# Optimization experiments

Hardware: AMD Instinct MI355X
Metric: run time of the kernel (lower is better)

The kernel has to match this reference:

```python
import jax, jax.numpy as jnp
import numpy as np

B, T, C, H = 2, 2048, 1024, 16
D = C // H  # head dim = 64
EPS = 1e-6  # kernel adds 1e-6 to softmax denominator


def setup_inputs() -> dict:
    key = jax.random.key(0)
    k1, k2, k3, k4, k5 = jax.random.split(key, 5)
    s = 1.0 / np.sqrt(C)
    return {
        "x": jax.random.normal(k1, (B, T, C), dtype=jnp.float32),
        "w_attn": jax.random.normal(k2, (3 * C, C), dtype=jnp.float32) * s,
        "b_attn": jax.random.normal(k3, (3 * C,), dtype=jnp.float32) * 0.02,
        "w_proj": jax.random.normal(k4, (C, C), dtype=jnp.float32) * s,
        "b_proj": jax.random.normal(k5, (C,), dtype=jnp.float32) * 0.02,
    }


def reference(x, w_attn, b_attn, w_proj, b_proj):
    b, t, c = x.shape
    qkv = x @ w_attn.T + b_attn                      # [B,T,3C]
    q, k, v = jnp.split(qkv, 3, axis=2)
    # [B,T,C] -> [B,H,T,D]
    q = q.reshape(b, t, H, D).transpose(0, 2, 1, 3)
    k = k.reshape(b, t, H, D).transpose(0, 2, 1, 3)
    v = v.reshape(b, t, H, D).transpose(0, 2, 1, 3)
    scale = 1.0 / np.sqrt(D)
    att = jnp.einsum("bhid,bhjd->bhij", q, k) * scale  # [B,H,T,T]
    causal = jnp.tril(jnp.ones((t, t), dtype=bool))
    att = jnp.where(causal, att, -jnp.inf)
    # softmax matching the HIP kernel: denom has +1e-6
    m = jnp.max(att, axis=-1, keepdims=True)
    e = jnp.exp(att - m)                             # masked entries -> 0
    p = e / (jnp.sum(e, axis=-1, keepdims=True) + EPS)
    y = jnp.einsum("bhij,bhjd->bhid", p, v)          # [B,H,T,D]
    y = y.transpose(0, 2, 1, 3).reshape(b, t, c)     # [B,T,C]
    return y @ w_proj.T + b_proj
```

## Files before the change

### kernel.cpp

```cpp
#include <hip/hip_runtime.h>

#define B_ 2
#define T_ 2048
#define C_ 1024
#define H_ 16
#define D_ 64

typedef __bf16 bf16x8 __attribute__((ext_vector_type(8)));
typedef float f32x4 __attribute__((ext_vector_type(4)));

__device__ __forceinline__ unsigned short f2bf(float f) {
  unsigned u = __float_as_uint(f);
  unsigned r = (u + 0x7fffu + ((u >> 16) & 1u)) >> 16;
  return (unsigned short)r;
}
__device__ __forceinline__ float bf2f(unsigned short u) {
  return __uint_as_float(((unsigned)u) << 16);
}

__global__ __launch_bounds__(256) void f32_to_bf16_kernel(
    const float* __restrict__ src, unsigned short* __restrict__ dst, int n4) {
  int i = blockIdx.x * 256 + threadIdx.x;
  if (i < n4) {
    float4 v = ((const float4*)src)[i];
    ushort4 u;
    u.x = f2bf(v.x); u.y = f2bf(v.y); u.z = f2bf(v.z); u.w = f2bf(v.w);
    ((ushort4*)dst)[i] = u;
  }
}

__global__ __launch_bounds__(256) void gemm_bt(
    const unsigned short* __restrict__ A,
    const unsigned short* __restrict__ Bm,
    const float* __restrict__ bias,
    int M, int N, int K, int mode,
    float* __restrict__ outf,
    unsigned short* __restrict__ qb,
    unsigned short* __restrict__ kb,
    unsigned short* __restrict__ vb) {
  __shared__ unsigned short As[128 * 64];
  __shared__ unsigned short Bs[128 * 64];

  const int tid  = threadIdx.x;
  const int lane = tid & 63;
  const int wave = tid >> 6;
  const int quad = lane >> 4;
  const int l16  = lane & 15;
  const int q4   = quad * 4;

  const int bm = blockIdx.y * 128;
  const int bn = blockIdx.x * 128;
  const int wm = (wave >> 1) * 64;
  const int wn = (wave & 1) * 64;

  f32x4 acc[4][4] = {};

  const int srow8 = lane >> 3;
  const int scol  = ((lane & 7) ^ srow8) * 8;
  const int srow  = wave * 8 + srow8;

  for (int k0 = 0; k0 < K; k0 += 64) {
#pragma unroll
    for (int c = 0; c < 4; ++c) {
      const int r = c * 32 + srow;
      const unsigned short* ga = A  + (size_t)(bm + r) * K + (k0 + scol);
      const unsigned short* gb = Bm + (size_t)(bn + r) * K + (k0 + scol);
      unsigned short* la = &As[(c * 32 + wave * 8) * 64];
      unsigned short* lb = &Bs[(c * 32 + wave * 8) * 64];
      __builtin_amdgcn_global_load_lds(
          (__attribute__((address_space(1))) unsigned int*)ga,
          (__attribute__((address_space(3))) unsigned int*)la, 16, 0, 0);
      __builtin_amdgcn_global_load_lds(
          (__attribute__((address_space(1))) unsigned int*)gb,
          (__attribute__((address_space(3))) unsigned int*)lb, 16, 0, 0);
    }
    __syncthreads();
#pragma unroll
    for (int ks = 0; ks < 2; ++ks) {
      bf16x8 af[4], bfr[4];
#pragma unroll
      for (int i = 0; i < 4; ++i)
        af[i] = *(const bf16x8*)&As[(wm + i * 16 + l16) * 64 +
                                    (((ks * 4 + quad) ^ (l16 & 7)) * 8)];
#pragma unroll
      for (int j = 0; j < 4; ++j)
        bfr[j] = *(const bf16x8*)&Bs[(wn + j * 16 + l16) * 64 +
                                     (((ks * 4 + quad) ^ (l16 & 7)) * 8)];
#pragma unroll
      for (int i = 0; i < 4; ++i)
#pragma unroll
        for (int j = 0; j < 4; ++j)
          acc[i][j] = __builtin_amdgcn_mfma_f32_16x16x32_bf16(af[i], bfr[j], acc[i][j], 0, 0, 0);
    }
    __syncthreads();
  }

#pragma unroll
  for (int j = 0; j < 4; ++j) {
    const int gn = bn + wn + j * 16 + l16;
    const float bv = bias[gn];
    if (mode == 0) {
#pragma unroll
      for (int i = 0; i < 4; ++i)
#pragma unroll
        for (int r = 0; r < 4; ++r) {
          const int gm = bm + wm + i * 16 + q4 + r;
          outf[(size_t)gm * N + gn] = acc[i][j][r] + bv;
        }
    } else {
      const int which = gn >> 10;
      const int cc = gn & 1023;
      const int h = cc >> 6, d = cc & 63;
      if (which == 2) {
#pragma unroll
        for (int i = 0; i < 4; ++i) {
          const int gm0 = bm + wm + i * 16 + q4;
          const int b = gm0 >> 11, t0 = gm0 & 2047;
          ushort4 u;
          u.x = f2bf(acc[i][j][0] + bv);
          u.y = f2bf(acc[i][j][1] + bv);
          u.z = f2bf(acc[i][j][2] + bv);
          u.w = f2bf(acc[i][j][3] + bv);
          *(ushort4*)&vb[(((size_t)(b * H_ + h) * D_) + d) * T_ + t0] = u;
        }
      } else {
        const float sc = (which == 0) ? 0.125f : 1.0f;
        unsigned short* dst = (which == 0) ? qb : kb;
#pragma unroll
        for (int i = 0; i < 4; ++i)
#pragma unroll
          for (int r = 0; r < 4; ++r) {
            const int gm = bm + wm + i * 16 + q4 + r;
            const int b = gm >> 11, t = gm & 2047;
            dst[(((size_t)(b * H_ + h) * T_) + t) * D_ + d] = f2bf((acc[i][j][r] + bv) * sc);
          }
      }
    }
  }
}

__global__ __launch_bounds__(256, 2) void attn_mfma(
    const unsigned short* __restrict__ Qb,
    const unsigned short* __restrict__ Kb,
    const unsigned short* __restrict__ Vtg,
    unsigned short* __restrict__ Yb) {
  __shared__ unsigned short Ks[64 * 64];
  __shared__ unsigned short Vt[64 * 64];
  __shared__ unsigned short Pw[4][32 * 64];

  const int tid  = threadIdx.x;
  const int lane = tid & 63;
  const int wave = tid >> 6;
  const int quad = lane >> 4;
  const int l16  = lane & 15;
  const int q4   = quad * 4;
  const int sw   = (l16 & 7);

  const int id = blockIdx.x;
  int bh, qt;
  if (id < 256) { bh = id & 31; qt = 15 - (id >> 5); }
  else          { bh = (id - 256) & 31; qt = (id - 256) >> 5; }
  const int b = bh >> 4, h = bh & 15;
  const size_t base = (size_t)bh * T_ * D_;

  const int wq = qt * 128 + wave * 32;

  bf16x8 qf[2][2];
#pragma unroll
  for (int nt = 0; nt < 2; ++nt)
#pragma unroll
    for (int ks = 0; ks < 2; ++ks)
      qf[nt][ks] = *(const bf16x8*)(Qb + base + (size_t)(wq + nt * 16 + l16) * 64 +
                                    ks * 32 + quad * 8);

  f32x4 o[4][2] = {};
  float l2[2] = {0.f, 0.f};

  const int ktiles = 2 * qt + 2;
  const int srow8 = lane >> 3;
  const int satom = ((lane & 7) ^ srow8) * 8;

  for (int kt = 0; kt < ktiles; ++kt) {
    const int kt0 = kt * 64;
    __syncthreads();
#pragma unroll
    for (int c = 0; c < 2; ++c) {
      const int row = wave * 16 + c * 8 + srow8;
      const unsigned short* gk = Kb  + base + (size_t)(kt0 + row) * 64 + satom;
      const unsigned short* gv = Vtg + base + (size_t)row * T_ + kt0 + satom;
      unsigned short* lk = &Ks[(wave * 16 + c * 8) * 64];
      unsigned short* lv = &Vt[(wave * 16 + c * 8) * 64];
      __builtin_amdgcn_global_load_lds(
          (__attribute__((address_space(1))) unsigned int*)gk,
          (__attribute__((address_space(3))) unsigned int*)lk, 16, 0, 0);
      __builtin_amdgcn_global_load_lds(
          (__attribute__((address_space(1))) unsigned int*)gv,
          (__attribute__((address_space(3))) unsigned int*)lv, 16, 0, 0);
    }
    __syncthreads();

    if (kt0 <= wq + 31) {
      f32x4 s[4][2] = {};
#pragma unroll
      for (int ks = 0; ks < 2; ++ks) {
        bf16x8 kf[4];
#pragma unroll
        for (int mt = 0; mt < 4; ++mt)
          kf[mt] = *(const bf16x8*)&Ks[(mt * 16 + l16) * 64 +
                                       (((ks * 4 + quad) ^ sw) * 8)];
#pragma unroll
        for (int mt = 0; mt < 4; ++mt)
#pragma unroll
          for (int nt = 0; nt < 2; ++nt)
            s[mt][nt] = __builtin_amdgcn_mfma_f32_16x16x32_bf16(kf[mt], qf[nt][ks],
                                                                s[mt][nt], 0, 0, 0);
      }
      if (kt0 + 63 > wq) {
#pragma unroll
        for (int mt = 0; mt < 4; ++mt)
#pragma unroll
          for (int nt = 0; nt < 2; ++nt)
#pragma unroll
            for (int r = 0; r < 4; ++r)
              if (kt0 + mt * 16 + q4 + r > wq + nt * 16 + l16) s[mt][nt][r] = -1e30f;
      }
#pragma unroll
      for (int nt = 0; nt < 2; ++nt) {
        float ps = 0.f;
#pragma unroll
        for (int mt = 0; mt < 4; ++mt) {
          float p0 = __expf(s[mt][nt][0]);
          float p1 = __expf(s[mt][nt][1]);
          float p2 = __expf(s[mt][nt][2]);
          float p3 = __expf(s[mt][nt][3]);
          ps += (p0 + p1) + (p2 + p3);
          unsigned lo = (unsigned)f2bf(p0) | ((unsigned)f2bf(p1) << 16);
          unsigned hi = (unsigned)f2bf(p2) | ((unsigned)f2bf(p3) << 16);
          uint2 pk; pk.x = lo; pk.y = hi;
          const int atom = (2 * mt + (quad >> 1)) ^ sw;
          *(uint2*)&Pw[wave][(nt * 16 + l16) * 64 + atom * 8 + (quad & 1) * 4] = pk;
        }
        l2[nt] += ps;
      }
#pragma unroll
      for (int ks = 0; ks < 2; ++ks) {
        bf16x8 vf[4], pf[2];
#pragma unroll
        for (int dt = 0; dt < 4; ++dt)
          vf[dt] = *(const bf16x8*)&Vt[(dt * 16 + l16) * 64 +
                                       (((ks * 4 + quad) ^ sw) * 8)];
#pragma unroll
        for (int nt = 0; nt < 2; ++nt)
          pf[nt] = *(const bf16x8*)&Pw[wave][(nt * 16 + l16) * 64 +
                                            (((ks * 4 + quad) ^ sw) * 8)];
#pragma unroll
        for (int dt = 0; dt < 4; ++dt)
#pragma unroll
          for (int nt = 0; nt < 2; ++nt)
            o[dt][nt] = __builtin_amdgcn_mfma_f32_16x16x32_bf16(vf[dt], pf[nt],
                                                                o[dt][nt], 0, 0, 0);
      }
    }
  }

#pragma unroll
  for (int nt = 0; nt < 2; ++nt) {
    float l = l2[nt];
    l += __shfl_xor(l, 16);
    l += __shfl_xor(l, 32);
    const float inv = 1.f / (l + 1e-6f);
    const int q = wq + nt * 16 + l16;
#pragma unroll
    for (int dt = 0; dt < 4; ++dt) {
      ushort4 u;
      u.x = f2bf(o[dt][nt][0] * inv);
      u.y = f2bf(o[dt][nt][1] * inv);
      u.z = f2bf(o[dt][nt][2] * inv);
      u.w = f2bf(o[dt][nt][3] * inv);
      *(ushort4*)&Yb[((size_t)(b * T_ + q)) * C_ + h * 64 + dt * 16 + q4] = u;
    }
  }
}

extern "C" void kernel_launch(void* const* d_in, const int* in_sizes, int n_in,
                              void* d_out, int out_size, void* d_ws, size_t ws_size,
                              hipStream_t stream) {
  const float* x      = (const float*)d_in[0];
  const float* w_attn = (const float*)d_in[1];
  const float* b_attn = (const float*)d_in[2];
  const float* w_proj = (const float*)d_in[3];
  const float* b_proj = (const float*)d_in[4];
  float* out = (float*)d_out;

  char* ws = (char*)d_ws;
  unsigned short* xb  = (unsigned short*)ws;  ws += (size_t)4096 * 1024 * 2;
  unsigned short* wab = (unsigned short*)ws;  ws += (size_t)3072 * 1024 * 2;
  unsigned short* wpb = (unsigned short*)ws;  ws += (size_t)1024 * 1024 * 2;
  unsigned short* qb  = (unsigned short*)ws;  ws += (size_t)B_ * H_ * T_ * D_ * 2;
  unsigned short* kb  = (unsigned short*)ws;  ws += (size_t)B_ * H_ * T_ * D_ * 2;
  unsigned short* vb  = (unsigned short*)ws;  ws += (size_t)B_ * H_ * T_ * D_ * 2;
  unsigned short* yb  = (unsigned short*)ws;  ws += (size_t)4096 * 1024 * 2;
  (void)ws_size; (void)in_sizes; (void)n_in; (void)out_size;

  f32_to_bf16_kernel<<<4096, 256, 0, stream>>>(x, xb, 1048576);
  f32_to_bf16_kernel<<<3072, 256, 0, stream>>>(w_attn, wab, 786432);
  f32_to_bf16_kernel<<<1024, 256, 0, stream>>>(w_proj, wpb, 262144);

  gemm_bt<<<dim3(24, 32), 256, 0, stream>>>(xb, wab, b_attn, 4096, 3072, 1024, 1,
                                            nullptr, qb, kb, vb);
  attn_mfma<<<512, 256, 0, stream>>>(qb, kb, vb, yb);
  gemm_bt<<<dim3(8, 32), 256, 0, stream>>>(yb, wpb, b_proj, 4096, 1024, 1024, 0,
                                           out, nullptr, nullptr, nullptr);
}
```

Measured before the change: 187.7 us.

## Use single-wave attention blocks and merge the three fp32-to-bf16 conversion launches

Restructures the attention kernel so each workgroup is one wave owning 32 query rows, with 2048 blocks instead of 512 four-wave blocks. Each wave loads its own K/V tiles and waits with s_waitcnt instead of block barriers, and its tile count is trimmed to the causal range. This removes __syncthreads and the idle waves on the diagonal, at the cost of four times more K/V global traffic per query tile and less LDS reuse. It also folds the three conversion kernels into one launch to cut launch overhead.

```diff
diff --git a/kernel.cpp b/kernel.cpp
--- a/kernel.cpp
+++ b/kernel.cpp
@@ -14,19 +14,23 @@
   unsigned r = (u + 0x7fffu + ((u >> 16) & 1u)) >> 16;
   return (unsigned short)r;
 }
-__device__ __forceinline__ float bf2f(unsigned short u) {
-  return __uint_as_float(((unsigned)u) << 16);
-}
-
-__global__ __launch_bounds__(256) void f32_to_bf16_kernel(
-    const float* __restrict__ src, unsigned short* __restrict__ dst, int n4) {
+
+#define NX 1048576
+#define NWA 786432
+#define NWP 262144
+__global__ __launch_bounds__(256) void convert_all(
+    const float* __restrict__ x, const float* __restrict__ wa,
+    const float* __restrict__ wp, unsigned short* __restrict__ xb,
+    unsigned short* __restrict__ wab, unsigned short* __restrict__ wpb) {
   int i = blockIdx.x * 256 + threadIdx.x;
-  if (i < n4) {
-    float4 v = ((const float4*)src)[i];
-    ushort4 u;
-    u.x = f2bf(v.x); u.y = f2bf(v.y); u.z = f2bf(v.z); u.w = f2bf(v.w);
-    ((ushort4*)dst)[i] = u;
-  }
+  const float* s; unsigned short* d; int j;
+  if (i < NX)            { s = x;  d = xb;  j = i; }
+  else if (i < NX + NWA) { s = wa; d = wab; j = i - NX; }
+  else                   { s = wp; d = wpb; j = i - NX - NWA; }
+  float4 v = ((const float4*)s)[j];
+  ushort4 u;
+  u.x = f2bf(v.x); u.y = f2bf(v.y); u.z = f2bf(v.z); u.w = f2bf(v.w);
+  ((ushort4*)d)[j] = u;
 }
 
 __global__ __launch_bounds__(256) void gemm_bt(
@@ -139,31 +143,28 @@
   }
 }
 
-__global__ __launch_bounds__(256, 2) void attn_mfma(
+__global__ __launch_bounds__(64) void attn_mfma(
     const unsigned short* __restrict__ Qb,
     const unsigned short* __restrict__ Kb,
     const unsigned short* __restrict__ Vtg,
     unsigned short* __restrict__ Yb) {
   __shared__ unsigned short Ks[64 * 64];
   __shared__ unsigned short Vt[64 * 64];
-  __shared__ unsigned short Pw[4][32 * 64];
-
-  const int tid  = threadIdx.x;
-  const int lane = tid & 63;
-  const int wave = tid >> 6;
+  __shared__ unsigned short Pw[32 * 64];
+
+  const int lane = threadIdx.x;
   const int quad = lane >> 4;
   const int l16  = lane & 15;
   const int q4   = quad * 4;
   const int sw   = (l16 & 7);
 
   const int id = blockIdx.x;
-  int bh, qt;
-  if (id < 256) { bh = id & 31; qt = 15 - (id >> 5); }
-  else          { bh = (id - 256) & 31; qt = (id - 256) >> 5; }
+  int bh, qs;
+  if (id < 1024) { bh = id & 31; qs = 63 - (id >> 5); }
+  else           { bh = (id - 1024) & 31; qs = (id - 1024) >> 5; }
   const int b = bh >> 4, h = bh & 15;
   const size_t base = (size_t)bh * T_ * D_;
-
-  const int wq = qt * 128 + wave * 32;
+  const int wq = qs * 32;
 
   bf16x8 qf[2][2];
 #pragma unroll
@@ -176,90 +177,85 @@
   f32x4 o[4][2] = {};
   float l2[2] = {0.f, 0.f};
 
-  const int ktiles = 2 * qt + 2;
+  const int ktiles = (qs * 32 + 95) >> 6;
   const int srow8 = lane >> 3;
   const int satom = ((lane & 7) ^ srow8) * 8;
 
   for (int kt = 0; kt < ktiles; ++kt) {
     const int kt0 = kt * 64;
-    __syncthreads();
-#pragma unroll
-    for (int c = 0; c < 2; ++c) {
-      const int row = wave * 16 + c * 8 + srow8;
+#pragma unroll
+    for (int c = 0; c < 8; ++c) {
+      const int row = c * 8 + srow8;
       const unsigned short* gk = Kb  + base + (size_t)(kt0 + row) * 64 + satom;
       const unsigned short* gv = Vtg + base + (size_t)row * T_ + kt0 + satom;
-      unsigned short* lk = &Ks[(wave * 16 + c * 8) * 64];
-      unsigned short* lv = &Vt[(wave * 16 + c * 8) * 64];
       __builtin_amdgcn_global_load_lds(
           (__attribute__((address_space(1))) unsigned int*)gk,
-          (__attribute__((address_space(3))) unsigned int*)lk, 16, 0, 0);
+          (__attribute__((address_space(3))) unsigned int*)&Ks[(c * 8) * 64], 16, 0, 0);
       __builtin_amdgcn_global_load_lds(
           (__attribute__((address_space(1))) unsigned int*)gv,
-          (__attribute__((address_space(3))) unsigned int*)lv, 16, 0, 0);
-    }
-    __syncthreads();
-
-    if (kt0 <= wq + 31) {
-      f32x4 s[4][2] = {};
-#pragma unroll
-      for (int ks = 0; ks < 2; ++ks) {
-        bf16x8 kf[4];
-#pragma unroll
-        for (int mt = 0; mt < 4; ++mt)
-          kf[mt] = *(const bf16x8*)&Ks[(mt * 16 + l16) * 64 +
-                                       (((ks * 4 + quad) ^ sw) * 8)];
-#pragma unroll
-        for (int mt = 0; mt < 4; ++mt)
-#pragma unroll
-          for (int nt = 0; nt < 2; ++nt)
-            s[mt][nt] = __builtin_amdgcn_mfma_f32_16x16x32_bf16(kf[mt], qf[nt][ks],
-                                                                s[mt][nt], 0, 0, 0);
+          (__attribute__((address_space(3))) unsigned int*)&Vt[(c * 8) * 64], 16, 0, 0);
+    }
+    __builtin_amdgcn_s_waitcnt(0x0F70);
+
+    f32x4 s[4][2] = {};
+#pragma unroll
+    for (int ks = 0; ks < 2; ++ks) {
+      bf16x8 kf[4];
+#pragma unroll
+      for (int mt = 0; mt < 4; ++mt)
+        kf[mt] = *(const bf16x8*)&Ks[(mt * 16 + l16) * 64 +
+                                     (((ks * 4 + quad) ^ sw) * 8)];
+#pragma unroll
+      for (int mt = 0; mt < 4; ++mt)
+#pragma unroll
+        for (int nt = 0; nt < 2; ++nt)
+          s[mt][nt] = __builtin_amdgcn_mfma_f32_16x16x32_bf16(kf[mt], qf[nt][ks],
+                                                              s[mt][nt], 0, 0, 0);
+    }
+    if (kt0 + 63 > wq) {
+#pragma unroll
+      for (int mt = 0; mt < 4; ++mt)
+#pragma unroll
+        for (int nt = 0; nt < 2; ++nt)
+#pragma unroll
+          for (int r = 0; r < 4; ++r)
+            if (kt0 + mt * 16 + q4 + r > wq + nt * 16 + l16) s[mt][nt][r] = -1e30f;
+    }
+#pragma unroll
+    for (int nt = 0; nt < 2; ++nt) {
+      float ps = 0.f;
+#pragma unroll
+      for (int mt = 0; mt < 4; ++mt) {
+        float p0 = __expf(s[mt][nt][0]);
+        float p1 = __expf(s[mt][nt][1]);
+        float p2 = __expf(s[mt][nt][2]);
+        float p3 = __expf(s[mt][nt][3]);
+        ps += (p0 + p1) + (p2 + p3);
+        unsigned lo = (unsigned)f2bf(p0) | ((unsigned)f2bf(p1) << 16);
+        unsigned hi = (unsigned)f2bf(p2) | ((unsigned)f2bf(p3) << 16);
+        uint2 pk; pk.x = lo; pk.y = hi;
+        const int atom = (2 * mt + (quad >> 1)) ^ sw;
+        *(uint2*)&Pw[(nt * 16 + l16) * 64 + atom * 8 + (quad & 1) * 4] = pk;
       }
-      if (kt0 + 63 > wq) {
-#pragma unroll
-        for (int mt = 0; mt < 4; ++mt)
-#pragma unroll
-          for (int nt = 0; nt < 2; ++nt)
-#pragma unroll
-            for (int r = 0; r < 4; ++r)
-              if (kt0 + mt * 16 + q4 + r > wq + nt * 16 + l16) s[mt][nt][r] = -1e30f;
-      }
-#pragma unroll
-      for (int nt = 0; nt < 2; ++nt) {
-        float ps = 0.f;
-#pragma unroll
-        for (int mt = 0; mt < 4; ++mt) {
-          float p0 = __expf(s[mt][nt][0]);
-          float p1 = __expf(s[mt][nt][1]);
-          float p2 = __expf(s[mt][nt][2]);
-          float p3 = __expf(s[mt][nt][3]);
-          ps += (p0 + p1) + (p2 + p3);
-          unsigned lo = (unsigned)f2bf(p0) | ((unsigned)f2bf(p1) << 16);
-          unsigned hi = (unsigned)f2bf(p2) | ((unsigned)f2bf(p3) << 16);
-          uint2 pk; pk.x = lo; pk.y = hi;
-          const int atom = (2 * mt + (quad >> 1)) ^ sw;
-          *(uint2*)&Pw[wave][(nt * 16 + l16) * 64 + atom * 8 + (quad & 1) * 4] = pk;
-        }
-        l2[nt] += ps;
-      }
-#pragma unroll
-      for (int ks = 0; ks < 2; ++ks) {
-        bf16x8 vf[4], pf[2];
-#pragma unroll
-        for (int dt = 0; dt < 4; ++dt)
-          vf[dt] = *(const bf16x8*)&Vt[(dt * 16 + l16) * 64 +
-                                       (((ks * 4 + quad) ^ sw) * 8)];
+      l2[nt] += ps;
+    }
+#pragma unroll
+    for (int ks = 0; ks < 2; ++ks) {
+      bf16x8 vf[4], pf[2];
+#pragma unroll
+      for (int dt = 0; dt < 4; ++dt)
+        vf[dt] = *(const bf16x8*)&Vt[(dt * 16 + l16) * 64 +
+                                     (((ks * 4 + quad) ^ sw) * 8)];
+#pragma unroll
+      for (int nt = 0; nt < 2; ++nt)
+        pf[nt] = *(const bf16x8*)&Pw[(nt * 16 + l16) * 64 +
+                                     (((ks * 4 + quad) ^ sw) * 8)];
+#pragma unroll
+      for (int dt = 0; dt < 4; ++dt)
 #pragma unroll
         for (int nt = 0; nt < 2; ++nt)
-          pf[nt] = *(const bf16x8*)&Pw[wave][(nt * 16 + l16) * 64 +
-                                            (((ks * 4 + quad) ^ sw) * 8)];
-#pragma unroll
-        for (int dt = 0; dt < 4; ++dt)
-#pragma unroll
-          for (int nt = 0; nt < 2; ++nt)
-            o[dt][nt] = __builtin_amdgcn_mfma_f32_16x16x32_bf16(vf[dt], pf[nt],
-                                                                o[dt][nt], 0, 0, 0);
-      }
+          o[dt][nt] = __builtin_amdgcn_mfma_f32_16x16x32_bf16(vf[dt], pf[nt],
+                                                              o[dt][nt], 0, 0, 0);
     }
   }
 
@@ -302,13 +298,11 @@
   unsigned short* yb  = (unsigned short*)ws;  ws += (size_t)4096 * 1024 * 2;
   (void)ws_size; (void)in_sizes; (void)n_in; (void)out_size;
 
-  f32_to_bf16_kernel<<<4096, 256, 0, stream>>>(x, xb, 1048576);
-  f32_to_bf16_kernel<<<3072, 256, 0, stream>>>(w_attn, wab, 786432);
-  f32_to_bf16_kernel<<<1024, 256, 0, stream>>>(w_proj, wpb, 262144);
+  convert_all<<<8192, 256, 0, stream>>>(x, w_attn, w_proj, xb, wab, wpb);
 
   gemm_bt<<<dim3(24, 32), 256, 0, stream>>>(xb, wab, b_attn, 4096, 3072, 1024, 1,
                                             nullptr, qb, kb, vb);
-  attn_mfma<<<512, 256, 0, stream>>>(qb, kb, vb, yb);
+  attn_mfma<<<2048, 64, 0, stream>>>(qb, kb, vb, yb);
   gemm_bt<<<dim3(8, 32), 256, 0, stream>>>(yb, wpb, b_proj, 4096, 1024, 1024, 0,
                                            out, nullptr, nullptr, nullptr);
 }
```

New measurement: 195.6 us. +4.2%, slower.

## Split causal attention KV range across blocks and add combine kernel

Applied to the files above, without the earlier changes.

Attention work per (batch, head) is split into 40 blocks. Longer query tiles get 2 to 4 KV chunks, each written as an unnormalized bf16 partial with its row sum, and a new combine kernel adds the partials and normalizes. The goal is to balance the causal triangle's uneven load and fill more CUs. The three f32-to-bf16 conversion launches are merged into one, and the P bf16 packing uses a cheaper perm-based rounding. The cost is extra global traffic, an extra launch, and bf16 rounding of the partials; the softmax has no max subtraction, so splitting does not change the numerics.

```diff
diff --git a/kernel.cpp b/kernel.cpp
--- a/kernel.cpp
+++ b/kernel.cpp
@@ -14,19 +14,23 @@
   unsigned r = (u + 0x7fffu + ((u >> 16) & 1u)) >> 16;
   return (unsigned short)r;
 }
-__device__ __forceinline__ float bf2f(unsigned short u) {
-  return __uint_as_float(((unsigned)u) << 16);
-}
-
-__global__ __launch_bounds__(256) void f32_to_bf16_kernel(
-    const float* __restrict__ src, unsigned short* __restrict__ dst, int n4) {
+
+#define NX 1048576
+#define NWA 786432
+#define NWP 262144
+__global__ __launch_bounds__(256) void convert_all(
+    const float* __restrict__ x, const float* __restrict__ wa,
+    const float* __restrict__ wp, unsigned short* __restrict__ xb,
+    unsigned short* __restrict__ wab, unsigned short* __restrict__ wpb) {
   int i = blockIdx.x * 256 + threadIdx.x;
-  if (i < n4) {
-    float4 v = ((const float4*)src)[i];
-    ushort4 u;
-    u.x = f2bf(v.x); u.y = f2bf(v.y); u.z = f2bf(v.z); u.w = f2bf(v.w);
-    ((ushort4*)dst)[i] = u;
-  }
+  const float* s; unsigned short* d; int j;
+  if (i < NX)            { s = x;  d = xb;  j = i; }
+  else if (i < NX + NWA) { s = wa; d = wab; j = i - NX; }
+  else                   { s = wp; d = wpb; j = i - NX - NWA; }
+  float4 v = ((const float4*)s)[j];
+  ushort4 u;
+  u.x = f2bf(v.x); u.y = f2bf(v.y); u.z = f2bf(v.z); u.w = f2bf(v.w);
+  ((ushort4*)d)[j] = u;
 }
 
 __global__ __launch_bounds__(256) void gemm_bt(
@@ -143,7 +147,9 @@
     const unsigned short* __restrict__ Qb,
     const unsigned short* __restrict__ Kb,
     const unsigned short* __restrict__ Vtg,
-    unsigned short* __restrict__ Yb) {
+    unsigned short* __restrict__ Yb,
+    unsigned short* __restrict__ op,
+    float* __restrict__ lp) {
   __shared__ unsigned short Ks[64 * 64];
   __shared__ unsigned short Vt[64 * 64];
   __shared__ unsigned short Pw[4][32 * 64];
@@ -157,13 +163,23 @@
   const int sw   = (l16 & 7);
 
   const int id = blockIdx.x;
-  int bh, qt;
-  if (id < 256) { bh = id & 31; qt = 15 - (id >> 5); }
-  else          { bh = (id - 256) & 31; qt = (id - 256) >> 5; }
+  const int bh = id / 40;
+  const int w  = id - bh * 40;
+  int qt, chunk, nsplits;
+  if (w < 4)       { qt = w;                 chunk = 0;            nsplits = 1; }
+  else if (w < 12) { qt = 4 + ((w - 4) >> 1); chunk = (w - 4) & 1;  nsplits = 2; }
+  else if (w < 24) { qt = 8 + (w - 12) / 3;  chunk = (w - 12) % 3; nsplits = 3; }
+  else             { qt = 12 + ((w - 24) >> 2); chunk = (w - 24) & 3; nsplits = 4; }
+
+  const int tiles_total = 2 * qt + 2;
+  const int tpc = (tiles_total + nsplits - 1) / nsplits;
+  const int t0 = chunk * tpc;
+  const int t1 = min(t0 + tpc, tiles_total);
+
   const int b = bh >> 4, h = bh & 15;
   const size_t base = (size_t)bh * T_ * D_;
-
   const int wq = qt * 128 + wave * 32;
+  const int wt1 = min(t1, (wq + 95) >> 6);
 
   bf16x8 qf[2][2];
 #pragma unroll
@@ -176,11 +192,10 @@
   f32x4 o[4][2] = {};
   float l2[2] = {0.f, 0.f};
 
-  const int ktiles = 2 * qt + 2;
   const int srow8 = lane >> 3;
   const int satom = ((lane & 7) ^ srow8) * 8;
 
-  for (int kt = 0; kt < ktiles; ++kt) {
+  for (int kt = t0; kt < t1; ++kt) {
     const int kt0 = kt * 64;
     __syncthreads();
 #pragma unroll
@@ -199,7 +214,7 @@
     }
     __syncthreads();
 
-    if (kt0 <= wq + 31) {
+    if (kt < wt1) {
       f32x4 s[4][2] = {};
 #pragma unroll
       for (int ks = 0; ks < 2; ++ks) {
@@ -234,8 +249,12 @@
           float p2 = __expf(s[mt][nt][2]);
           float p3 = __expf(s[mt][nt][3]);
           ps += (p0 + p1) + (p2 + p3);
-          unsigned lo = (unsigned)f2bf(p0) | ((unsigned)f2bf(p1) << 16);
-          unsigned hi = (unsigned)f2bf(p2) | ((unsigned)f2bf(p3) << 16);
+          unsigned lo = __builtin_amdgcn_perm(__float_as_uint(p1) + 0x8000u,
+                                              __float_as_uint(p0) + 0x8000u,
+                                              0x07060302u);
+          unsigned hi = __builtin_amdgcn_perm(__float_as_uint(p3) + 0x8000u,
+                                              __float_as_uint(p2) + 0x8000u,
+                                              0x07060302u);
           uint2 pk; pk.x = lo; pk.y = hi;
           const int atom = (2 * mt + (quad >> 1)) ^ sw;
           *(uint2*)&Pw[wave][(nt * 16 + l16) * 64 + atom * 8 + (quad & 1) * 4] = pk;
@@ -268,17 +287,84 @@
     float l = l2[nt];
     l += __shfl_xor(l, 16);
     l += __shfl_xor(l, 32);
-    const float inv = 1.f / (l + 1e-6f);
-    const int q = wq + nt * 16 + l16;
-#pragma unroll
-    for (int dt = 0; dt < 4; ++dt) {
-      ushort4 u;
-      u.x = f2bf(o[dt][nt][0] * inv);
-      u.y = f2bf(o[dt][nt][1] * inv);
-      u.z = f2bf(o[dt][nt][2] * inv);
-      u.w = f2bf(o[dt][nt][3] * inv);
-      *(ushort4*)&Yb[((size_t)(b * T_ + q)) * C_ + h * 64 + dt * 16 + q4] = u;
-    }
+    const int qloc = wave * 32 + nt * 16 + l16;
+    if (nsplits == 1) {
+      const float inv = 1.f / (l + 1e-6f);
+      const int q = qt * 128 + qloc;
+#pragma unroll
+      for (int dt = 0; dt < 4; ++dt) {
+        ushort4 u;
+        u.x = f2bf(o[dt][nt][0] * inv);
+        u.y = f2bf(o[dt][nt][1] * inv);
+        u.z = f2bf(o[dt][nt][2] * inv);
+        u.w = f2bf(o[dt][nt][3] * inv);
+        *(ushort4*)&Yb[((size_t)(b * T_ + q)) * C_ + h * 64 + dt * 16 + q4] = u;
+      }
+    } else {
+      if (quad == 0) lp[(size_t)id * 128 + qloc] = l;
+#pragma unroll
+      for (int dt = 0; dt < 4; ++dt) {
+        ushort4 u;
+        u.x = f2bf(o[dt][nt][0]);
+        u.y = f2bf(o[dt][nt][1]);
+        u.z = f2bf(o[dt][nt][2]);
+        u.w = f2bf(o[dt][nt][3]);
+        *(ushort4*)&op[(size_t)id * 8192 + (size_t)qloc * 64 + dt * 16 + q4] = u;
+      }
+    }
+  }
+}
+
+__global__ __launch_bounds__(256) void attn_combine(
+    const unsigned short* __restrict__ op, const float* __restrict__ lp,
+    unsigned short* __restrict__ Yb) {
+  const int cb = blockIdx.x;
+  const int bh = cb / 12;
+  const int qi = cb - bh * 12;
+  const int qt = 4 + qi;
+  int nsplits, pfx;
+  if (qt < 8)       { nsplits = 2; pfx = 4 + 2 * (qt - 4); }
+  else if (qt < 12) { nsplits = 3; pfx = 12 + 3 * (qt - 8); }
+  else              { nsplits = 4; pfx = 24 + 4 * (qt - 12); }
+  const int slot0 = bh * 40 + pfx;
+
+  const int t = threadIdx.x;
+  const int qloc = t >> 1;
+  const int d0 = (t & 1) * 32;
+
+  float l = 1e-6f;
+  float acc[32];
+#pragma unroll
+  for (int i = 0; i < 32; ++i) acc[i] = 0.f;
+  for (int s = 0; s < nsplits; ++s) {
+    l += lp[(size_t)(slot0 + s) * 128 + qloc];
+    const uint4* src = (const uint4*)(op + (size_t)(slot0 + s) * 8192 +
+                                      (size_t)qloc * 64 + d0);
+#pragma unroll
+    for (int c = 0; c < 4; ++c) {
+      uint4 v = src[c];
+      acc[c*8+0] += __uint_as_float(v.x << 16);
+      acc[c*8+1] += __uint_as_float(v.x & 0xffff0000u);
+      acc[c*8+2] += __uint_as_float(v.y << 16);
+      acc[c*8+3] += __uint_as_float(v.y & 0xffff0000u);
+      acc[c*8+4] += __uint_as_float(v.z << 16);
+      acc[c*8+5] += __uint_as_float(v.z & 0xffff0000u);
+      acc[c*8+6] += __uint_as_float(v.w << 16);
+      acc[c*8+7] += __uint_as_float(v.w & 0xffff0000u);
+    }
+  }
+  const float inv = 1.f / l;
+  const int b = bh >> 4, h = bh & 15;
+  const int q = qt * 128 + qloc;
+  uint4* dst = (uint4*)(Yb + ((size_t)(b * T_ + q)) * C_ + h * 64 + d0);
+#pragma unroll
+  for (int c = 0; c < 4; ++c) {
+    uint4 v;
+    v.x = (unsigned)f2bf(acc[c*8+0] * inv) | ((unsigned)f2bf(acc[c*8+1] * inv) << 16);
+    v.y = (unsigned)f2bf(acc[c*8+2] * inv) | ((unsigned)f2bf(acc[c*8+3] * inv) << 16);
+    v.z = (unsigned)f2bf(acc[c*8+4] * inv) | ((unsigned)f2bf(acc[c*8+5] * inv) << 16);
+    v.w = (unsigned)f2bf(acc[c*8+6] * inv) | ((unsigned)f2bf(acc[c*8+7] * inv) << 16);
+    dst[c] = v;
   }
 }
 
@@ -300,15 +386,16 @@
   unsigned short* kb  = (unsigned short*)ws;  ws += (size_t)B_ * H_ * T_ * D_ * 2;
   unsigned short* vb  = (unsigned short*)ws;  ws += (size_t)B_ * H_ * T_ * D_ * 2;
   unsigned short* yb  = (unsigned short*)ws;  ws += (size_t)4096 * 1024 * 2;
+  unsigned short* op  = (unsigned short*)ws;  ws += (size_t)1280 * 128 * 64 * 2;
+  float*          lp  = (float*)ws;           ws += (size_t)1280 * 128 * 4;
   (void)ws_size; (void)in_sizes; (void)n_in; (void)out_size;
 
-  f32_to_bf16_kernel<<<4096, 256, 0, stream>>>(x, xb, 1048576);
-  f32_to_bf16_kernel<<<3072, 256, 0, stream>>>(w_attn, wab, 786432);
-  f32_to_bf16_kernel<<<1024, 256, 0, stream>>>(w_proj, wpb, 262144);
+  convert_all<<<8192, 256, 0, stream>>>(x, w_attn, w_proj, xb, wab, wpb);
 
   gemm_bt<<<dim3(24, 32), 256, 0, stream>>>(xb, wab, b_attn, 4096, 3072, 1024, 1,
                                             nullptr, qb, kb, vb);
-  attn_mfma<<<512, 256, 0, stream>>>(qb, kb, vb, yb);
+  attn_mfma<<<1280, 256, 0, stream>>>(qb, kb, vb, yb, op, lp);
+  attn_combine<<<384, 256, 0, stream>>>(op, lp, yb);
   gemm_bt<<<dim3(8, 32), 256, 0, stream>>>(yb, wpb, b_proj, 4096, 1024, 1024, 0,
                                            out, nullptr, nullptr, nullptr);
 }
```

After: 183.4 us. 1.02x faster.
